# Optimization experiments

Measured on AMD Instinct MI355X. Metric: run time of the kernel, lower is better.

The kernel has to match this reference:

```python
import jax, jax.numpy as jnp
import numpy as np

N = 8192          # number of priors
TOP_K = 50        # max detections returned
IOU_THR = 0.3     # NMS IoU threshold (module-level constant)
VAR0, VAR1 = 0.1, 0.2  # variance buffer


def setup_inputs() -> dict:
    key = jax.random.key(0)
    k1, k2, k3, k4, k5 = jax.random.split(key, 5)
    loc = jax.random.normal(k1, (N, 14), jnp.float32)
    conf = jax.random.uniform(k2, (N, 2), jnp.float32)
    # some iou scores slightly out of [0,1] to exercise the clamp
    iou = jax.random.uniform(k3, (N, 1), jnp.float32) * 1.2 - 0.1
    cxcy = jax.random.uniform(k4, (N, 2), jnp.float32)            # anchor centers in [0,1)
    wh = jax.random.uniform(k5, (N, 2), jnp.float32) * 0.19 + 0.01  # anchor sizes in (0.01,0.2)
    priors = jnp.concatenate([cxcy, wh], axis=1)
    return {"loc": loc, "conf": conf, "iou": iou, "priors": priors}


def _decode(loc, conf, iou, priors):
    cls_scores = conf[:, 1]
    iou_scores = jnp.clip(iou[:, 0], 0.0, 1.0)
    scores = jnp.sqrt(cls_scores * iou_scores)
    p_cxcy, p_wh = priors[:, 0:2], priors[:, 2:4]
    bb_cxcy = p_cxcy + loc[:, 0:2] * VAR0 * p_wh
    var = jnp.array([VAR0, VAR1], jnp.float32)
    bb_wh_half = p_wh * jnp.exp(loc[:, 2:4] * var) * 0.5
    bboxes = jnp.concatenate([bb_cxcy - bb_wh_half, bb_cxcy + bb_wh_half], axis=1)
    # 5 landmarks, each decoded like the box center
    lms = jnp.concatenate(
        [p_cxcy + loc[:, 4 + 2 * i:6 + 2 * i] * VAR0 * p_wh for i in range(5)], axis=1)
    return bboxes, lms, scores


def _nms_keep_idx(bboxes, scores):
    """Greedy NMS; returns indices (into original order) of the first TOP_K kept boxes."""
    order = jnp.argsort(-scores)
    b = bboxes[order]
    x1, y1, x2, y2 = b[:, 0], b[:, 1], b[:, 2], b[:, 3]
    area = (x2 - x1) * (y2 - y1)
    iw = jnp.maximum(jnp.minimum(x2[:, None], x2[None, :]) - jnp.maximum(x1[:, None], x1[None, :]), 0.0)
    ih = jnp.maximum(jnp.minimum(y2[:, None], y2[None, :]) - jnp.maximum(y1[:, None], y1[None, :]), 0.0)
    inter = iw * ih
    iou_mat = inter / (area[:, None] + area[None, :] - inter)  # [N, N]
    idxs = jnp.arange(N)

    def body(i, keep):
        suppressed = jnp.any((iou_mat[i] > IOU_THR) & keep & (idxs < i))
        return keep.at[i].set(~suppressed)

    keep = jax.lax.fori_loop(0, N, body, jnp.zeros((N,), bool))
    kept_pos = jnp.nonzero(keep, size=TOP_K, fill_value=0)[0]  # fixed-size under jit
    return order[kept_pos]


def reference(loc, conf, iou, priors):
    bboxes, lms, scores = _decode(loc, conf, iou, priors)
    keep_idx = _nms_keep_idx(bboxes, scores)
    dets = jnp.concatenate(
        [bboxes[keep_idx], lms[keep_idx], scores[keep_idx][:, None]], axis=1)  # [TOP_K, 15]
    return dets
```

## Files before the change

kernel.cpp:

```cpp
#include <hip/hip_runtime.h>

#define NBOX 8192
#define TOP_K 50
#define IOU_THR 0.3f
#define VAR0 0.1f
#define VAR1 0.2f
#define NT 512
#define NWAVE (NT / 64)
#define MSEL 128
#define PRE_MAX 256
#define BPT 16

__device__ __forceinline__ void decode_box(int cidx, const float* __restrict__ loc,
                                           const float* __restrict__ priors,
                                           float& x1, float& y1, float& x2, float& y2,
                                           float& area)
{
    float4 pr = *reinterpret_cast<const float4*>(priors + 4 * cidx);
    float l0 = loc[cidx * 14 + 0];
    float l1 = loc[cidx * 14 + 1];
    float l2 = loc[cidx * 14 + 2];
    float l3 = loc[cidx * 14 + 3];
    float cx = pr.x + l0 * VAR0 * pr.z;
    float cy = pr.y + l1 * VAR0 * pr.w;
    float hw = pr.z * expf(l2 * VAR0) * 0.5f;
    float hh = pr.w * expf(l3 * VAR1) * 0.5f;
    x1 = cx - hw; y1 = cy - hh; x2 = cx + hw; y2 = cy + hh;
    area = (x2 - x1) * (y2 - y1);
}

__device__ __forceinline__ void find_thresh(unsigned c0, unsigned c1, unsigned c2, unsigned c3,
                                            unsigned base_above, int lane,
                                            int& bin_sel, unsigned& above_sel)
{
    unsigned cnt = c0 + c1 + c2 + c3;
    unsigned S = cnt;
    #pragma unroll
    for (int d = 1; d < 64; d <<= 1) {
        unsigned t = __shfl_down(S, d);
        if (lane + d < 64) S += t;
    }
    unsigned long long bal = __ballot(base_above + S >= MSEL);
    int lstar = 63 - __clzll(bal);
    int src = (lstar < 63) ? (lstar + 1) : lstar;
    unsigned Snext = __shfl(S, src);
    unsigned above = base_above + ((lstar < 63) ? Snext : 0u);
    unsigned bl[4] = {c0, c1, c2, c3};
    int bsel = -1; unsigned abv = above; unsigned acc = above;
    #pragma unroll
    for (int k = 3; k >= 0; --k) {
        if (bsel < 0) {
            if (acc + bl[k] >= MSEL) { bsel = k; abv = acc; }
            else acc += bl[k];
        }
    }
    bin_sel  = 4 * lstar + __shfl(bsel, lstar);
    above_sel = __shfl(abv, lstar);
}

__device__ void bitonic_sort(unsigned long long* a, int S, int tid)
{
    for (int k = 2; k <= S; k <<= 1) {
        for (int j = k >> 1; j > 0; j >>= 1) {
            __syncthreads();
            for (int i = tid; i < S; i += NT) {
                int l = i ^ j;
                if (l > i) {
                    unsigned long long A = a[i];
                    unsigned long long B = a[l];
                    bool asc = ((i & k) == 0);
                    if ((A > B) == asc) { a[i] = B; a[l] = A; }
                }
            }
        }
    }
    __syncthreads();
}

__device__ int greedy_nms_serial(const unsigned long long* __restrict__ arr, int n, int lane,
                                 const float* __restrict__ loc, const float* __restrict__ priors,
                                 int* keep_out)
{
    float kx1 = 0.f, ky1 = 0.f, kx2 = 0.f, ky2 = 0.f, karea = 0.f;
    int my_keep = 0, idx0 = 0, kept = 0;
    bool done = false;
    for (int p = 0; p < n && !done; p += 64) {
        int cidx = 0;
        float x1 = 0.f, y1 = 0.f, x2 = 0.f, y2 = 0.f, area = 0.f;
        int pos = p + lane;
        if (pos < n) {
            cidx = (int)(arr[pos] & 0xFFFFFFFFull);
            decode_box(cidx, loc, priors, x1, y1, x2, y2, area);
        }
        int nb = (n - p) < 64 ? (n - p) : 64;
        for (int c = 0; c < nb; ++c) {
            float bx1 = __shfl(x1, c);
            float by1 = __shfl(y1, c);
            float bx2 = __shfl(x2, c);
            float by2 = __shfl(y2, c);
            float barea = __shfl(area, c);
            int   bidx  = __shfl(cidx, c);
            float iw = fmaxf(fminf(kx2, bx2) - fmaxf(kx1, bx1), 0.0f);
            float ih = fmaxf(fminf(ky2, by2) - fmaxf(ky1, by1), 0.0f);
            float inter = iw * ih;
            float v = inter / (karea + barea - inter);
            bool sup = (lane < kept) && (v > IOU_THR);
            if (__ballot(sup) == 0ull) {
                if (kept == 0) idx0 = bidx;
                if (lane == kept) {
                    kx1 = bx1; ky1 = by1; kx2 = bx2; ky2 = by2; karea = barea;
                    my_keep = bidx;
                }
                ++kept;
                if (kept == TOP_K) { done = true; break; }
            }
        }
    }
    if (lane < TOP_K) keep_out[lane] = (lane < kept) ? my_keep : idx0;
    return kept;
}

__global__ __launch_bounds__(NT) void yunet_fused_kernel(
    const float* __restrict__ loc,
    const float* __restrict__ conf,
    const float* __restrict__ iou,
    const float* __restrict__ priors,
    float* __restrict__ out)
{
    __shared__ unsigned long long keys[NBOX];
    __shared__ unsigned long long cand[PRE_MAX];
    __shared__ unsigned hist[NWAVE][256] __attribute__((aligned(16)));
    __shared__ unsigned long long maskbuf[64];
    __shared__ unsigned long long sh_supprev;
    __shared__ float4 boxs4[PRE_MAX];
    __shared__ float  boxsa[PRE_MAX];
    __shared__ float4 keptb4[TOP_K];
    __shared__ float  kepta[TOP_K];
    __shared__ int keep_sh[TOP_K];
    __shared__ unsigned sh_cnt;
    __shared__ int sh_flag, sh_kept;

    const int tid = threadIdx.x;
    const int lane = tid & 63;

    const float4* conf4 = reinterpret_cast<const float4*>(conf);
    const float4* iou4  = reinterpret_cast<const float4*>(iou);
    float4 cf[8], io[4];
    #pragma unroll
    for (int m = 0; m < 2; ++m)
        #pragma unroll
        for (int q = 0; q < 4; ++q)
            cf[m * 4 + q] = conf4[(m * NT + tid) * 4 + q];
    #pragma unroll
    for (int m = 0; m < 2; ++m)
        #pragma unroll
        for (int r = 0; r < 2; ++r)
            io[m * 2 + r] = iou4[(m * NT + tid) * 2 + r];

    {
        unsigned* hz = &hist[0][0];
        for (int i = tid; i < NWAVE * 256; i += NT) hz[i] = 0;
        if (tid == 0) { sh_cnt = 0; sh_flag = 0; sh_kept = 0; }
    }
    __syncthreads();

    unsigned sbv[BPT];
    #pragma unroll
    for (int m = 0; m < 2; ++m) {
        float sc[8], uu[8];
        #pragma unroll
        for (int q = 0; q < 4; ++q) {
            sc[2 * q]     = cf[m * 4 + q].y;
            sc[2 * q + 1] = cf[m * 4 + q].w;
        }
        #pragma unroll
        for (int r = 0; r < 2; ++r) {
            uu[4 * r + 0] = io[m * 2 + r].x; uu[4 * r + 1] = io[m * 2 + r].y;
            uu[4 * r + 2] = io[m * 2 + r].z; uu[4 * r + 3] = io[m * 2 + r].w;
        }
        #pragma unroll
        for (int q = 0; q < 8; ++q) {
            float u = fminf(fmaxf(uu[q], 0.0f), 1.0f);
            float s = sqrtf(sc[q] * u);
            unsigned sb = __float_as_uint(s);
            sbv[m * 8 + q] = sb;
            int bin = (int)(s * 256.0f); bin = bin > 255 ? 255 : bin;
            atomicAdd(&hist[tid >> 6][bin], 1u);
        }
    }
    __syncthreads();

    int B;
    {
        unsigned c0 = 0, c1 = 0, c2 = 0, c3 = 0;
        #pragma unroll
        for (int w = 0; w < NWAVE; ++w) {
            uint4 h = *(const uint4*)&hist[w][4 * lane];
            c0 += h.x; c1 += h.y; c2 += h.z; c3 += h.w;
        }
        unsigned ab;
        find_thresh(c0, c1, c2, c3, 0u, lane, B, ab);
    }

    #pragma unroll
    for (int m = 0; m < 2; ++m) {
        #pragma unroll
        for (int q = 0; q < 8; ++q) {
            unsigned sb = sbv[m * 8 + q];
            float s = __uint_as_float(sb);
            int bin = (int)(s * 256.0f); bin = bin > 255 ? 255 : bin;
            if (bin >= B) {
                unsigned pos = atomicAdd(&sh_cnt, 1u);
                if (pos < PRE_MAX)
                    cand[pos] = ((unsigned long long)(~sb) << 32)
                              | (unsigned)((m * NT + tid) * 8 + q);
            }
        }
    }
    __syncthreads();
    const int C = (int)sh_cnt;

    if (C <= PRE_MAX) {
        if (tid < C) {
            unsigned long long k = cand[tid];
            int r = 0, j = 0;
            for (; j + 4 <= C; j += 4) {
                r += (cand[j]     < k) ? 1 : 0;
                r += (cand[j + 1] < k) ? 1 : 0;
                r += (cand[j + 2] < k) ? 1 : 0;
                r += (cand[j + 3] < k) ? 1 : 0;
            }
            for (; j < C; ++j) r += (cand[j] < k) ? 1 : 0;
            keys[r] = k;
            int cidx = (int)(k & 0xFFFFFFFFull);
            float x1, y1, x2, y2, area;
            decode_box(cidx, loc, priors, x1, y1, x2, y2, area);
            boxs4[r] = make_float4(x1, y1, x2, y2);
            boxsa[r] = area;
        }
        __syncthreads();

        for (int p = 0; p < C; p += 64) {
            if (tid < 64) {
                int pos = p + lane;
                bool valid = pos < C;
                int rp = valid ? pos : 0;
                float4 b = boxs4[rp]; float a = boxsa[rp];
                int kept = sh_kept;
                bool supP = !valid;
                for (int j = 0; j < kept; ++j) {
                    float4 kb = keptb4[j]; float ka = kepta[j];
                    float iw = fmaxf(fminf(b.z, kb.z) - fmaxf(b.x, kb.x), 0.f);
                    float ih = fmaxf(fminf(b.w, kb.w) - fmaxf(b.y, kb.y), 0.f);
                    float inter = iw * ih;
                    supP = supP || (inter > IOU_THR * (a + ka - inter));
                }
                unsigned long long sp = __ballot(supP);
                if (lane == 0) sh_supprev = sp;
            }
            __syncthreads();

            {
                int r  = tid >> 3;
                int cb = tid & 7;
                int rp = (p + r < C) ? p + r : 0;
                float4 rb = boxs4[rp]; float ra = boxsa[rp];
                unsigned byte = 0;
                #pragma unroll
                for (int k = 0; k < 8; ++k) {
                    int c = cb * 8 + k;
                    int cp = (p + c < C) ? p + c : 0;
                    float4 cx = boxs4[cp]; float ca = boxsa[cp];
                    float iw = fmaxf(fminf(rb.z, cx.z) - fmaxf(rb.x, cx.x), 0.f);
                    float ih = fmaxf(fminf(rb.w, cx.w) - fmaxf(rb.y, cx.y), 0.f);
                    float inter = iw * ih;
                    byte |= (unsigned)((inter > IOU_THR * (ra + ca - inter)) ? 1u : 0u) << k;
                }
                ((unsigned char*)maskbuf)[tid] = (unsigned char)byte;
            }
            __syncthreads();

            if (tid < 64) {
                unsigned long long mymask = maskbuf[lane];
                unsigned long long sup_prev = sh_supprev;
                unsigned long long keepcur = 0ull;
                const int kept0 = sh_kept;
                int kept = kept0;
                for (int i2 = 0; i2 < 64 && kept < TOP_K; ++i2) {
                    unsigned long long mi = __shfl(mymask, i2);
                    unsigned long long lower = (1ull << i2) - 1ull;
                    if (!((sup_prev >> i2) & 1ull) && !(mi & keepcur & lower)) {
                        keepcur |= 1ull << i2;
                        ++kept;
                    }
                }
                unsigned long long lowm = (1ull << lane) - 1ull;
                int rank = kept0 + __popcll(keepcur & lowm);
                if (((keepcur >> lane) & 1ull) && rank < TOP_K) {
                    int pos = p + lane;
                    keep_sh[rank] = (int)(keys[pos] & 0xFFFFFFFFull);
                    keptb4[rank] = boxs4[pos];
                    kepta[rank] = boxsa[pos];
                }
                if (lane == 0) sh_kept = kept;
            }
            __syncthreads();
            if (sh_kept >= TOP_K) break;
        }
        if (tid == 0) sh_flag = (sh_kept >= TOP_K) ? 0 : 1;
    } else {
        if (tid == 0) sh_flag = 1;
    }
    __syncthreads();

    if (sh_flag) {
        #pragma unroll
        for (int m = 0; m < 2; ++m) {
            #pragma unroll
            for (int q = 0; q < 8; ++q) {
                int i = (m * NT + tid) * 8 + q;
                keys[i] = ((unsigned long long)(~sbv[m * 8 + q]) << 32) | (unsigned)i;
            }
        }
        __syncthreads();
        bitonic_sort(keys, NBOX, tid);
        if (tid < 64) greedy_nms_serial(keys, NBOX, tid, loc, priors, keep_sh);
        if (tid == 0) sh_kept = TOP_K;
        __syncthreads();
    }

    if (tid < TOP_K) {
        int src = (tid < sh_kept) ? tid : 0;
        int i = keep_sh[src];
        float4 pr = *reinterpret_cast<const float4*>(priors + 4 * i);
        float cx = pr.x + loc[i * 14 + 0] * VAR0 * pr.z;
        float cy = pr.y + loc[i * 14 + 1] * VAR0 * pr.w;
        float hw = pr.z * expf(loc[i * 14 + 2] * VAR0) * 0.5f;
        float hh = pr.w * expf(loc[i * 14 + 3] * VAR1) * 0.5f;
        float* o = out + tid * 15;
        o[0] = cx - hw;
        o[1] = cy - hh;
        o[2] = cx + hw;
        o[3] = cy + hh;
        #pragma unroll
        for (int q = 0; q < 5; ++q) {
            o[4 + 2 * q] = pr.x + loc[i * 14 + 4 + 2 * q] * VAR0 * pr.z;
            o[5 + 2 * q] = pr.y + loc[i * 14 + 5 + 2 * q] * VAR0 * pr.w;
        }
        float cc = conf[i * 2 + 1];
        float u  = fminf(fmaxf(iou[i], 0.0f), 1.0f);
        o[14] = sqrtf(cc * u);
    }
}

extern "C" void kernel_launch(void* const* d_in, const int* in_sizes, int n_in,
                              void* d_out, int out_size, void* d_ws, size_t ws_size,
                              hipStream_t stream) {
    const float* loc    = (const float*)d_in[0];
    const float* conf   = (const float*)d_in[1];
    const float* iou    = (const float*)d_in[2];
    const float* priors = (const float*)d_in[3];
    float* out = (float*)d_out;

    yunet_fused_kernel<<<1, NT, 0, stream>>>(loc, conf, iou, priors, out);
}
```

Measured before the change: 23.18 us.

## Run post-selection NMS on a single wavefront to drop block barriers

After candidate selection, only wave 0 continues. It does the rank sort, the IoU mask build and the greedy sweep with LDS waitcnts in place of __syncthreads, and reads mask bits through readlane instead of a shared mask buffer. Candidate compaction switches to a ballot-aggregated atomic, one per wave instead of one per element. The mask and rank work that all 512 threads used to share is now serialized on 64 lanes. The fallback bitonic sort also runs on one wave, so that path becomes much slower.

Measured after the change: 33.21 us. 43.3% more time.

```diff
diff --git a/kernel.cpp b/kernel.cpp
--- a/kernel.cpp
+++ b/kernel.cpp
@@ -10,6 +10,8 @@
 #define MSEL 128
 #define PRE_MAX 256
 #define BPT 16
+
+#define WAITLDS() __asm__ volatile("s_waitcnt lgkmcnt(0)" ::: "memory")
 
 __device__ __forceinline__ void decode_box(int cidx, const float* __restrict__ loc,
                                            const float* __restrict__ priors,
@@ -30,8 +32,7 @@
 }
 
 __device__ __forceinline__ void find_thresh(unsigned c0, unsigned c1, unsigned c2, unsigned c3,
-                                            unsigned base_above, int lane,
-                                            int& bin_sel, unsigned& above_sel)
+                                            int lane, int& bin_sel)
 {
     unsigned cnt = c0 + c1 + c2 + c3;
     unsigned S = cnt;
@@ -40,30 +41,29 @@
         unsigned t = __shfl_down(S, d);
         if (lane + d < 64) S += t;
     }
-    unsigned long long bal = __ballot(base_above + S >= MSEL);
+    unsigned long long bal = __ballot(S >= MSEL);
     int lstar = 63 - __clzll(bal);
     int src = (lstar < 63) ? (lstar + 1) : lstar;
     unsigned Snext = __shfl(S, src);
-    unsigned above = base_above + ((lstar < 63) ? Snext : 0u);
+    unsigned above = (lstar < 63) ? Snext : 0u;
     unsigned bl[4] = {c0, c1, c2, c3};
-    int bsel = -1; unsigned abv = above; unsigned acc = above;
+    int bsel = -1; unsigned acc = above;
     #pragma unroll
     for (int k = 3; k >= 0; --k) {
         if (bsel < 0) {
-            if (acc + bl[k] >= MSEL) { bsel = k; abv = acc; }
+            if (acc + bl[k] >= MSEL) bsel = k;
             else acc += bl[k];
         }
     }
-    bin_sel  = 4 * lstar + __shfl(bsel, lstar);
-    above_sel = __shfl(abv, lstar);
-}
-
-__device__ void bitonic_sort(unsigned long long* a, int S, int tid)
+    bin_sel = 4 * lstar + __shfl(bsel, lstar);
+}
+
+__device__ void bitonic_sort_w0(unsigned long long* a, int S, int lane)
 {
     for (int k = 2; k <= S; k <<= 1) {
         for (int j = k >> 1; j > 0; j >>= 1) {
-            __syncthreads();
-            for (int i = tid; i < S; i += NT) {
+            WAITLDS();
+            for (int i = lane; i < S; i += 64) {
                 int l = i ^ j;
                 if (l > i) {
                     unsigned long long A = a[i];
@@ -74,12 +74,12 @@
             }
         }
     }
-    __syncthreads();
-}
-
-__device__ int greedy_nms_serial(const unsigned long long* __restrict__ arr, int n, int lane,
-                                 const float* __restrict__ loc, const float* __restrict__ priors,
-                                 int* keep_out)
+    WAITLDS();
+}
+
+__device__ void greedy_nms_serial(const unsigned long long* __restrict__ arr, int n, int lane,
+                                  const float* __restrict__ loc, const float* __restrict__ priors,
+                                  int* keep_out)
 {
     float kx1 = 0.f, ky1 = 0.f, kx2 = 0.f, ky2 = 0.f, karea = 0.f;
     int my_keep = 0, idx0 = 0, kept = 0;
@@ -117,7 +117,6 @@
         }
     }
     if (lane < TOP_K) keep_out[lane] = (lane < kept) ? my_keep : idx0;
-    return kept;
 }
 
 __global__ __launch_bounds__(NT) void yunet_fused_kernel(
@@ -130,18 +129,16 @@
     __shared__ unsigned long long keys[NBOX];
     __shared__ unsigned long long cand[PRE_MAX];
     __shared__ unsigned hist[NWAVE][256] __attribute__((aligned(16)));
-    __shared__ unsigned long long maskbuf[64];
-    __shared__ unsigned long long sh_supprev;
     __shared__ float4 boxs4[PRE_MAX];
     __shared__ float  boxsa[PRE_MAX];
     __shared__ float4 keptb4[TOP_K];
     __shared__ float  kepta[TOP_K];
     __shared__ int keep_sh[TOP_K];
     __shared__ unsigned sh_cnt;
-    __shared__ int sh_flag, sh_kept;
-
-    const int tid = threadIdx.x;
+
+    const int tid  = threadIdx.x;
     const int lane = tid & 63;
+    const int wid  = tid >> 6;
 
     const float4* conf4 = reinterpret_cast<const float4*>(conf);
     const float4* iou4  = reinterpret_cast<const float4*>(iou);
@@ -157,12 +154,10 @@
         for (int r = 0; r < 2; ++r)
             io[m * 2 + r] = iou4[(m * NT + tid) * 2 + r];
 
-    {
-        unsigned* hz = &hist[0][0];
-        for (int i = tid; i < NWAVE * 256; i += NT) hz[i] = 0;
-        if (tid == 0) { sh_cnt = 0; sh_flag = 0; sh_kept = 0; }
-    }
-    __syncthreads();
+    #pragma unroll
+    for (int i = 0; i < 4; ++i) hist[wid][lane + 64 * i] = 0;
+    if (tid == 0) sh_cnt = 0;
+    WAITLDS();
 
     unsigned sbv[BPT];
     #pragma unroll
@@ -185,7 +180,7 @@
             unsigned sb = __float_as_uint(s);
             sbv[m * 8 + q] = sb;
             int bin = (int)(s * 256.0f); bin = bin > 255 ? 255 : bin;
-            atomicAdd(&hist[tid >> 6][bin], 1u);
+            atomicAdd(&hist[wid][bin], 1u);
         }
     }
     __syncthreads();
@@ -198,8 +193,7 @@
             uint4 h = *(const uint4*)&hist[w][4 * lane];
             c0 += h.x; c1 += h.y; c2 += h.z; c3 += h.w;
         }
-        unsigned ab;
-        find_thresh(c0, c1, c2, c3, 0u, lane, B, ab);
+        find_thresh(c0, c1, c2, c3, lane, B);
     }
 
     #pragma unroll
@@ -209,8 +203,14 @@
             unsigned sb = sbv[m * 8 + q];
             float s = __uint_as_float(sb);
             int bin = (int)(s * 256.0f); bin = bin > 255 ? 255 : bin;
-            if (bin >= B) {
-                unsigned pos = atomicAdd(&sh_cnt, 1u);
+            bool pred = (bin >= B);
+            unsigned long long bal = __ballot(pred);
+            if (pred) {
+                int myoff = __popcll(bal & ((1ull << lane) - 1ull));
+                unsigned base = 0;
+                if (myoff == 0) base = atomicAdd(&sh_cnt, (unsigned)__popcll(bal));
+                base = (unsigned)__builtin_amdgcn_readfirstlane((int)base);
+                unsigned pos = base + (unsigned)myoff;
                 if (pos < PRE_MAX)
                     cand[pos] = ((unsigned long long)(~sb) << 32)
                               | (unsigned)((m * NT + tid) * 8 + q);
@@ -220,9 +220,13 @@
     __syncthreads();
     const int C = (int)sh_cnt;
 
-    if (C <= PRE_MAX) {
-        if (tid < C) {
-            unsigned long long k = cand[tid];
+    if (wid != 0) return;
+
+    bool need_fallback = (C > PRE_MAX);
+
+    if (!need_fallback) {
+        for (int i = lane; i < C; i += 64) {
+            unsigned long long k = cand[i];
             int r = 0, j = 0;
             for (; j + 4 <= C; j += 4) {
                 r += (cand[j]     < k) ? 1 : 0;
@@ -231,113 +235,87 @@
                 r += (cand[j + 3] < k) ? 1 : 0;
             }
             for (; j < C; ++j) r += (cand[j] < k) ? 1 : 0;
-            keys[r] = k;
             int cidx = (int)(k & 0xFFFFFFFFull);
             float x1, y1, x2, y2, area;
             decode_box(cidx, loc, priors, x1, y1, x2, y2, area);
+            keys[r] = k;
             boxs4[r] = make_float4(x1, y1, x2, y2);
             boxsa[r] = area;
         }
-        __syncthreads();
-
-        for (int p = 0; p < C; p += 64) {
-            if (tid < 64) {
-                int pos = p + lane;
-                bool valid = pos < C;
-                int rp = valid ? pos : 0;
-                float4 b = boxs4[rp]; float a = boxsa[rp];
-                int kept = sh_kept;
-                bool supP = !valid;
-                for (int j = 0; j < kept; ++j) {
-                    float4 kb = keptb4[j]; float ka = kepta[j];
-                    float iw = fmaxf(fminf(b.z, kb.z) - fmaxf(b.x, kb.x), 0.f);
-                    float ih = fmaxf(fminf(b.w, kb.w) - fmaxf(b.y, kb.y), 0.f);
-                    float inter = iw * ih;
-                    supP = supP || (inter > IOU_THR * (a + ka - inter));
+        WAITLDS();
+
+        int kept = 0;
+        for (int p = 0; p < C && kept < TOP_K; p += 64) {
+            int pos = p + lane;
+            bool valid = pos < C;
+            int rp = valid ? pos : 0;
+            float4 b = boxs4[rp]; float a = boxsa[rp];
+
+            bool supP = !valid;
+            for (int j = 0; j < kept; ++j) {
+                float4 kb = keptb4[j]; float ka = kepta[j];
+                float iw = fmaxf(fminf(b.z, kb.z) - fmaxf(b.x, kb.x), 0.f);
+                float ih = fmaxf(fminf(b.w, kb.w) - fmaxf(b.y, kb.y), 0.f);
+                float inter = iw * ih;
+                supP = supP || (inter > IOU_THR * (a + ka - inter));
+            }
+            unsigned long long sup_prev = __ballot(supP);
+
+            unsigned mlo = 0u, mhi = 0u;
+            for (int j = 0; j < 64; ++j) {
+                int cp = (p + j < C) ? p + j : 0;
+                float4 cb = boxs4[cp]; float ca = boxsa[cp];
+                float iw = fmaxf(fminf(b.z, cb.z) - fmaxf(b.x, cb.x), 0.f);
+                float ih = fmaxf(fminf(b.w, cb.w) - fmaxf(b.y, cb.y), 0.f);
+                float inter = iw * ih;
+                unsigned bit = (inter > IOU_THR * (a + ca - inter)) ? 1u : 0u;
+                if (j < 32) mlo |= bit << j; else mhi |= bit << (j - 32);
+            }
+
+            unsigned long long keepcur = 0ull;
+            int kept0 = kept;
+            for (int j = 0; j < 64 && kept < TOP_K; ++j) {
+                if (!((sup_prev >> j) & 1ull)) {
+                    unsigned long long mj =
+                        ((unsigned long long)(unsigned)__builtin_amdgcn_readlane((int)mhi, j) << 32)
+                      | (unsigned)__builtin_amdgcn_readlane((int)mlo, j);
+                    unsigned long long lower = (1ull << j) - 1ull;
+                    if (!(mj & keepcur & lower)) { keepcur |= (1ull << j); ++kept; }
                 }
-                unsigned long long sp = __ballot(supP);
-                if (lane == 0) sh_supprev = sp;
-            }
-            __syncthreads();
-
-            {
-                int r  = tid >> 3;
-                int cb = tid & 7;
-                int rp = (p + r < C) ? p + r : 0;
-                float4 rb = boxs4[rp]; float ra = boxsa[rp];
-                unsigned byte = 0;
-                #pragma unroll
-                for (int k = 0; k < 8; ++k) {
-                    int c = cb * 8 + k;
-                    int cp = (p + c < C) ? p + c : 0;
-                    float4 cx = boxs4[cp]; float ca = boxsa[cp];
-                    float iw = fmaxf(fminf(rb.z, cx.z) - fmaxf(rb.x, cx.x), 0.f);
-                    float ih = fmaxf(fminf(rb.w, cx.w) - fmaxf(rb.y, cx.y), 0.f);
-                    float inter = iw * ih;
-                    byte |= (unsigned)((inter > IOU_THR * (ra + ca - inter)) ? 1u : 0u) << k;
-                }
-                ((unsigned char*)maskbuf)[tid] = (unsigned char)byte;
-            }
-            __syncthreads();
-
-            if (tid < 64) {
-                unsigned long long mymask = maskbuf[lane];
-                unsigned long long sup_prev = sh_supprev;
-                unsigned long long keepcur = 0ull;
-                const int kept0 = sh_kept;
-                int kept = kept0;
-                for (int i2 = 0; i2 < 64 && kept < TOP_K; ++i2) {
-                    unsigned long long mi = __shfl(mymask, i2);
-                    unsigned long long lower = (1ull << i2) - 1ull;
-                    if (!((sup_prev >> i2) & 1ull) && !(mi & keepcur & lower)) {
-                        keepcur |= 1ull << i2;
-                        ++kept;
-                    }
-                }
-                unsigned long long lowm = (1ull << lane) - 1ull;
+            }
+
+            unsigned long long lowm = (1ull << lane) - 1ull;
+            if ((keepcur >> lane) & 1ull) {
                 int rank = kept0 + __popcll(keepcur & lowm);
-                if (((keepcur >> lane) & 1ull) && rank < TOP_K) {
-                    int pos = p + lane;
-                    keep_sh[rank] = (int)(keys[pos] & 0xFFFFFFFFull);
-                    keptb4[rank] = boxs4[pos];
-                    kepta[rank] = boxsa[pos];
-                }
-                if (lane == 0) sh_kept = kept;
-            }
-            __syncthreads();
-            if (sh_kept >= TOP_K) break;
-        }
-        if (tid == 0) sh_flag = (sh_kept >= TOP_K) ? 0 : 1;
-    } else {
-        if (tid == 0) sh_flag = 1;
-    }
-    __syncthreads();
-
-    if (sh_flag) {
-        #pragma unroll
-        for (int m = 0; m < 2; ++m) {
-            #pragma unroll
-            for (int q = 0; q < 8; ++q) {
-                int i = (m * NT + tid) * 8 + q;
-                keys[i] = ((unsigned long long)(~sbv[m * 8 + q]) << 32) | (unsigned)i;
-            }
-        }
-        __syncthreads();
-        bitonic_sort(keys, NBOX, tid);
-        if (tid < 64) greedy_nms_serial(keys, NBOX, tid, loc, priors, keep_sh);
-        if (tid == 0) sh_kept = TOP_K;
-        __syncthreads();
-    }
-
-    if (tid < TOP_K) {
-        int src = (tid < sh_kept) ? tid : 0;
-        int i = keep_sh[src];
+                keep_sh[rank] = (int)(keys[pos] & 0xFFFFFFFFull);
+                keptb4[rank] = b;
+                kepta[rank] = a;
+            }
+            WAITLDS();
+        }
+        need_fallback = (kept < TOP_K);
+    }
+
+    if (need_fallback) {
+        for (int i = lane; i < NBOX; i += 64) {
+            float c = conf[2 * i + 1];
+            float u = fminf(fmaxf(iou[i], 0.f), 1.f);
+            float s = sqrtf(c * u);
+            keys[i] = ((unsigned long long)(~__float_as_uint(s)) << 32) | (unsigned)i;
+        }
+        bitonic_sort_w0(keys, NBOX, lane);
+        greedy_nms_serial(keys, NBOX, lane, loc, priors, keep_sh);
+        WAITLDS();
+    }
+
+    if (lane < TOP_K) {
+        int i = keep_sh[lane];
         float4 pr = *reinterpret_cast<const float4*>(priors + 4 * i);
         float cx = pr.x + loc[i * 14 + 0] * VAR0 * pr.z;
         float cy = pr.y + loc[i * 14 + 1] * VAR0 * pr.w;
         float hw = pr.z * expf(loc[i * 14 + 2] * VAR0) * 0.5f;
         float hh = pr.w * expf(loc[i * 14 + 3] * VAR1) * 0.5f;
-        float* o = out + tid * 15;
+        float* o = out + lane * 15;
         o[0] = cx - hw;
         o[1] = cy - hh;
         o[2] = cx + hw;
```
